# Kernel optimization log

Hardware: AMD Instinct MI355X
Metric: run time of the kernel (lower is better)

## Reference

```python
import jax, jax.numpy as jnp
import numpy as np

HEADS = 6
K = 3       # kernel_size
PAD = 1     # padding (stride = 1, so AvgPool is identity and h=H, w=W)


def setup_inputs() -> dict:
    key = jax.random.key(0)
    ks = jax.random.split(key, 6)
    B, H, W, C = 8, 56, 56, 192
    k4h = (K ** 4) * HEADS  # 486
    s = 0.02
    return {
        "x":  jax.random.normal(ks[0], (B, H, W, C), jnp.float32),
        # weights stored as (in, out), i.e. transpose of torch nn.Linear.weight
        "Wv": jax.random.normal(ks[1], (C, C), jnp.float32) * s,
        "Wa": jax.random.normal(ks[2], (C, k4h), jnp.float32) * s,
        "ba": jnp.zeros((k4h,), jnp.float32),
        "Wp": jax.random.normal(ks[3], (C, C), jnp.float32) * s,
        "bp": jnp.zeros((C,), jnp.float32),
    }


def _outlook(x, Wv, Wa, ba, Wp, bp):
    B, H, W, C = x.shape
    hd = C // HEADS
    scale = hd ** (-0.5)
    k2 = K * K
    hw = H * W

    # v projection (no bias), to NCHW
    v = jnp.einsum("bhwc,cd->bdhw", x, Wv)                       # [B,C,H,W]

    # unfold: extract k x k local windows (same ordering as nn.Unfold: C, ki, kj)
    vp = jnp.pad(v, ((0, 0), (0, 0), (PAD, PAD), (PAD, PAD)))
    patches = jnp.stack(
        [vp[:, :, i:i + H, j:j + W] for i in range(K) for j in range(K)],
        axis=2,
    )                                                            # [B,C,k2,H,W]
    v = patches.reshape(B, HEADS, hd, k2, hw).transpose(0, 1, 4, 3, 2)  # [B,h,hw,k2,hd]

    # attention weights: dense predicted per location (pool is identity, stride=1)
    a = x.reshape(B, hw, C) @ Wa + ba                            # [B,hw,heads*k2*k2]
    a = a.reshape(B, hw, HEADS, k2, k2).transpose(0, 2, 1, 3, 4)  # [B,h,hw,k2,k2]
    a = jax.nn.softmax(a * scale, axis=-1)

    out = jnp.einsum("bnpkq,bnpqd->bnpkd", a, v)                 # [B,h,hw,k2,hd]

    # fold (col2im): scatter-add overlapping windows back, stride=1
    cols = out.transpose(0, 1, 4, 3, 2).reshape(B, C, K, K, H, W)
    acc = jnp.zeros((B, C, H + 2 * PAD, W + 2 * PAD), x.dtype)
    for i in range(K):
        for j in range(K):
            acc = acc.at[:, :, i:i + H, j:j + W].add(cols[:, :, i, j])
    y = acc[:, :, PAD:PAD + H, PAD:PAD + W].transpose(0, 2, 3, 1)  # [B,H,W,C]

    return y @ Wp + bp


def reference(x, Wv, Wa, ba, Wp, bp):
    return _outlook(x, Wv, Wa, ba, Wp, bp)
```

## Files before the change

kernel.cpp:

```cpp
#include <hip/hip_runtime.h>
#include <hip/hip_bf16.h>
#include <cstdint>

#define DI __device__ __forceinline__

typedef __attribute__((ext_vector_type(8))) short short8;
typedef __attribute__((ext_vector_type(4))) float f32x4;

DI float bflo(uint32_t u) { return __builtin_bit_cast(float, (uint32_t)(u << 16)); }
DI float bfhi(uint32_t u) { return __builtin_bit_cast(float, (uint32_t)(u & 0xffff0000u)); }
DI float bf2f(uint16_t u) { return __builtin_bit_cast(float, (uint32_t)((uint32_t)u << 16)); }
DI uint16_t f2bf(float f) {
    uint32_t x = __builtin_bit_cast(uint32_t, f);
    x += 0x7fffu + ((x >> 16) & 1u);
    return (uint16_t)(x >> 16);
}
DI uint32_t pk2bf(float a, float b) {
    return (uint32_t)f2bf(a) | ((uint32_t)f2bf(b) << 16);
}

DI int xcd_swizzle(int orig, int nwg) {
    const int q = nwg >> 3, r = nwg & 7;
    const int x = orig & 7, i = orig >> 3;
    return (x < r ? x * (q + 1) : r * (q + 1) + (x - r) * q) + i;
}

constexpr int BATCH = 8, HH_IMG = 56, WW_IMG = 56, C = 192;
constexpr int HEADS = 6, HD = 32, NA = 486;
constexpr int MROWS = BATCH * HH_IMG * WW_IMG;
constexpr int KK = 192;

template <bool A_BF16, bool O0_BF16, int NT, int SPLIT>
__global__ __launch_bounds__(256) void gemm_tile(
    const void* __restrict__ Ap,
    const float* __restrict__ W0, int N0, void* __restrict__ out0,
    const float* __restrict__ bias0,
    const float* __restrict__ W1, int N1, uint16_t* __restrict__ out1,
    const float* __restrict__ bias1) {
    __shared__ __align__(16) uint8_t sm[49152];
    const int t    = threadIdx.x;
    const int wgid = xcd_swizzle(blockIdx.x, gridDim.x);
    const int mg   = wgid / NT, ti = wgid - mg * NT;
    const int m0   = mg * 128;
    const int l    = t & 63, wid = t >> 6;
    const int wr   = wid >> 1, wc = wid & 1;
    const int lr   = l & 15, lg = l >> 4;

    if (A_BF16) {
        const uint16_t* A = (const uint16_t*)Ap;
#pragma unroll
        for (int i = 0; i < 12; ++i) {
            const int f = t + i * 256;
            const int m = f / 24, cb = (f % 24) * 16;
            const uint4 val = *(const uint4*)(A + (size_t)(m0 + m) * KK + (cb >> 1));
            *(uint4*)(sm + m * 384 + (cb ^ ((m & 7) << 4))) = val;
        }
    } else {
        const float* A = (const float*)Ap;
#pragma unroll
        for (int i = 0; i < 12; ++i) {
            const int f = t + i * 256;
            const int m = f / 24, cb = (f % 24) * 16;
            const int k = cb >> 1;
            const float4 v0 = *(const float4*)(A + (size_t)(m0 + m) * KK + k);
            const float4 v1 = *(const float4*)(A + (size_t)(m0 + m) * KK + k + 4);
            uint4 o;
            o.x = pk2bf(v0.x, v0.y); o.y = pk2bf(v0.z, v0.w);
            o.z = pk2bf(v1.x, v1.y); o.w = pk2bf(v1.z, v1.w);
            *(uint4*)(sm + m * 384 + (cb ^ ((m & 7) << 4))) = o;
        }
    }
    __syncthreads();

    short8 aR[6][4];
#pragma unroll
    for (int ks = 0; ks < 6; ++ks)
#pragma unroll
        for (int mr = 0; mr < 4; ++mr) {
            const int row = wr * 64 + mr * 16 + lr;
            aR[ks][mr] = *(const short8*)(sm + row * 384 +
                          ((ks * 64 + lg * 16) ^ ((row & 7) << 4)));
        }
    __syncthreads();

    const bool  to0   = ti < SPLIT;
    const float* Ws   = to0 ? W0 : W1;
    const int   ncols = to0 ? N0 : N1;
    const int   bcol  = ti * 64 - (to0 ? 0 : N0);
    {
        const int bn = t & 63, kq = t >> 6;
        const int gn = bcol + bn;
        const bool valid = gn < ncols;
        uint8_t* buf = sm + bn * 384;
        const int sw = (bn & 7) << 4;
        const float* Wf = Ws + (size_t)(kq * 48) * ncols + gn;
#pragma unroll
        for (int e16 = 0; e16 < 6; ++e16) {
            uint32_t d[4];
#pragma unroll
            for (int p = 0; p < 4; ++p) {
                const int e = e16 * 4 + p;
                const float f0 = valid ? Wf[(size_t)(2 * e) * ncols]     : 0.f;
                const float f1 = valid ? Wf[(size_t)(2 * e + 1) * ncols] : 0.f;
                d[p] = pk2bf(f0, f1);
            }
            *(uint4*)(buf + ((kq * 96 + e16 * 16) ^ sw)) = make_uint4(d[0], d[1], d[2], d[3]);
        }
    }
    __syncthreads();

    f32x4 acc[4][2];
#pragma unroll
    for (int mr = 0; mr < 4; ++mr) {
        acc[mr][0] = f32x4{0.f, 0.f, 0.f, 0.f};
        acc[mr][1] = f32x4{0.f, 0.f, 0.f, 0.f};
    }
#pragma unroll
    for (int ks = 0; ks < 6; ++ks) {
        const int cb  = ks * 64 + lg * 16;
        const int rn0 = wc * 32 + lr, rn1 = rn0 + 16;
        const short8 b0 = *(const short8*)(sm + rn0 * 384 + (cb ^ ((rn0 & 7) << 4)));
        const short8 b1 = *(const short8*)(sm + rn1 * 384 + (cb ^ ((rn1 & 7) << 4)));
#pragma unroll
        for (int mr = 0; mr < 4; ++mr) {
            acc[mr][0] = __builtin_amdgcn_mfma_f32_16x16x32_bf16(aR[ks][mr], b0, acc[mr][0], 0, 0, 0);
            acc[mr][1] = __builtin_amdgcn_mfma_f32_16x16x32_bf16(aR[ks][mr], b1, acc[mr][1], 0, 0, 0);
        }
    }

    const float* bias = to0 ? bias0 : bias1;
#pragma unroll
    for (int nr = 0; nr < 2; ++nr) {
        const int col = bcol + wc * 32 + nr * 16 + lr;
        if (col < ncols) {
            const float bv = bias ? bias[col] : 0.f;
#pragma unroll
            for (int mr = 0; mr < 4; ++mr) {
                const size_t rowb = (size_t)(m0 + wr * 64 + mr * 16 + lg * 4);
#pragma unroll
                for (int j = 0; j < 4; ++j) {
                    const float val = acc[mr][nr][j] + bv;
                    if (to0) {
                        if (O0_BF16) ((uint16_t*)out0)[(rowb + j) * ncols + col] = f2bf(val);
                        else         ((float*)out0)[(rowb + j) * ncols + col]    = val;
                    } else {
                        out1[(rowb + j) * ncols + col] = f2bf(val);
                    }
                }
            }
        }
    }
}

constexpr int TH = 4, TW = 8;
constexpr int HALO_W = TW + 4;
constexpr int VSTR = C + 8;

__global__ __launch_bounds__(192) void attn_fold25(const uint16_t* __restrict__ v,
                                                   const uint16_t* __restrict__ alog,
                                                   uint16_t* __restrict__ ypre) {
    __shared__ uint16_t vl[96][VSTR];
    const int b   = blockIdx.z;
    const int ty0 = blockIdx.y * TH, tx0 = blockIdx.x * TW;
    const int t   = threadIdx.x;

#pragma unroll
    for (int it = 0; it < 12; ++it) {
        const int f  = t + it * 192;
        const int px = f / 24, c8 = (f % 24) * 8;
        const int hy = px / HALO_W, hx = px % HALO_W;
        const int y = ty0 + hy - 2, x = tx0 + hx - 2;
        uint4 val = make_uint4(0u, 0u, 0u, 0u);
        if ((unsigned)y < HH_IMG && (unsigned)x < WW_IMG)
            val = *(const uint4*)&v[(((size_t)b * HH_IMG + y) * WW_IMG + x) * C + c8];
        *(uint4*)&vl[px][c8] = val;
    }

    const int n   = t % HEADS, pxl = t / HEADS;
    const int py  = pxl / TW, px_ = pxl % TW;
    const int Py  = ty0 + py, Px = tx0 + px_;
    const float scale = 0.17677669529663687f;

    float cw[5][5] = {};
#pragma unroll
    for (int i = 0; i < 3; ++i)
#pragma unroll
        for (int j = 0; j < 3; ++j) {
            const int sy = Py - i + 1, sx = Px - j + 1;
            if ((unsigned)sy < HH_IMG && (unsigned)sx < WW_IMG) {
                const uint16_t* ap = alog + (((size_t)b * HH_IMG + sy) * WW_IMG + sx) * NA
                                   + n * 81 + (i * 3 + j) * 9;
                float L[9], mx = -1e30f;
#pragma unroll
                for (int q = 0; q < 9; ++q) { L[q] = bf2f(ap[q]) * scale; mx = fmaxf(mx, L[q]); }
                float w[9], s = 0.f;
#pragma unroll
                for (int q = 0; q < 9; ++q) { w[q] = __expf(L[q] - mx); s += w[q]; }
                const float inv = 1.f / s;
#pragma unroll
                for (int qi = 0; qi < 3; ++qi)
#pragma unroll
                    for (int qj = 0; qj < 3; ++qj)
                        cw[qi - i + 2][qj - j + 2] += w[qi * 3 + qj] * inv;
            }
        }
    __syncthreads();

    float acc[HD] = {};
#pragma unroll
    for (int dy = 0; dy < 5; ++dy)
#pragma unroll
        for (int dx = 0; dx < 5; ++dx) {
            const float wq = cw[dy][dx];
            const uint16_t* vp = &vl[(py + dy) * HALO_W + (px_ + dx)][n * HD];
#pragma unroll
            for (int v8 = 0; v8 < 4; ++v8) {
                const uint4 raw = *(const uint4*)&vp[v8 * 8];
                const uint32_t r0 = raw.x, r1 = raw.y, r2 = raw.z, r3 = raw.w;
                acc[v8*8+0] = fmaf(wq, bflo(r0), acc[v8*8+0]);
                acc[v8*8+1] = fmaf(wq, bfhi(r0), acc[v8*8+1]);
                acc[v8*8+2] = fmaf(wq, bflo(r1), acc[v8*8+2]);
                acc[v8*8+3] = fmaf(wq, bfhi(r1), acc[v8*8+3]);
                acc[v8*8+4] = fmaf(wq, bflo(r2), acc[v8*8+4]);
                acc[v8*8+5] = fmaf(wq, bfhi(r2), acc[v8*8+5]);
                acc[v8*8+6] = fmaf(wq, bflo(r3), acc[v8*8+6]);
                acc[v8*8+7] = fmaf(wq, bfhi(r3), acc[v8*8+7]);
            }
        }

    uint16_t* op = ypre + (((size_t)b * HH_IMG + Py) * WW_IMG + Px) * C + n * HD;
#pragma unroll
    for (int d = 0; d < HD; d += 2)
        *(uint32_t*)&op[d] = pk2bf(acc[d], acc[d + 1]);
}

extern "C" void kernel_launch(void* const* d_in, const int* in_sizes, int n_in,
                              void* d_out, int out_size, void* d_ws, size_t ws_size,
                              hipStream_t stream) {
    const float* x  = (const float*)d_in[0];
    const float* Wv = (const float*)d_in[1];
    const float* Wa = (const float*)d_in[2];
    const float* ba = (const float*)d_in[3];
    const float* Wp = (const float*)d_in[4];
    const float* bp = (const float*)d_in[5];
    float* out = (float*)d_out;

    uint16_t* v    = (uint16_t*)d_ws;
    uint16_t* alog = v + (size_t)MROWS * C;
    uint16_t* ypre = alog + (size_t)MROWS * NA;

    gemm_tile<false, true, 11, 3><<<(MROWS / 128) * 11, 256, 0, stream>>>(
        x, Wv, C, v, nullptr, Wa, NA, alog, ba);
    attn_fold25<<<dim3(WW_IMG / TW, HH_IMG / TH, BATCH), dim3(192), 0, stream>>>(
        v, alog, ypre);
    gemm_tile<true, false, 3, 3><<<(MROWS / 128) * 3, 256, 0, stream>>>(
        ypre, Wp, C, out, bp, nullptr, 0, nullptr, nullptr);
}
```

Measured before the change: 68.95 us.

## Pre-pack bf16 weight tiles, widen GEMM N-tile, use direct-to-LDS loads

A new prep kernel converts Wv/Wa/Wp once per call into pre-swizzled bf16 tiles in the workspace. The GEMMs then stream them with global_load_lds instead of strided fp32 gathers and per-thread conversion. The GEMM tile widens from 64 to 128 columns with 4x4 MFMA accumulators and paired-column packed stores. Hardware cvt_pk_bf16 replaces software rounding. Softmax drops the max subtraction and uses exp2/rcp intrinsics, and ypre is written pre-swizzled so the projection GEMM can load it straight into LDS. Risks are an extra launch, overflow if logits are large without the max subtraction, and higher register pressure.

```diff
diff --git a/kernel.cpp b/kernel.cpp
--- a/kernel.cpp
+++ b/kernel.cpp
@@ -10,13 +10,16 @@
 DI float bflo(uint32_t u) { return __builtin_bit_cast(float, (uint32_t)(u << 16)); }
 DI float bfhi(uint32_t u) { return __builtin_bit_cast(float, (uint32_t)(u & 0xffff0000u)); }
 DI float bf2f(uint16_t u) { return __builtin_bit_cast(float, (uint32_t)((uint32_t)u << 16)); }
-DI uint16_t f2bf(float f) {
-    uint32_t x = __builtin_bit_cast(uint32_t, f);
-    x += 0x7fffu + ((x >> 16) & 1u);
-    return (uint16_t)(x >> 16);
-}
-DI uint32_t pk2bf(float a, float b) {
-    return (uint32_t)f2bf(a) | ((uint32_t)f2bf(b) << 16);
+DI uint32_t cvtpk(float lo, float hi) {
+    uint32_t r;
+    asm("v_cvt_pk_bf16_f32 %0, %1, %2" : "=v"(r) : "v"(lo), "v"(hi));
+    return r;
+}
+
+DI void gload16(const void* g, void* s) {
+    __builtin_amdgcn_global_load_lds(
+        (const __attribute__((address_space(1))) uint32_t*)g,
+        (__attribute__((address_space(3))) uint32_t*)s, 16, 0, 0);
 }
 
 DI int xcd_swizzle(int orig, int nwg) {
@@ -29,15 +32,47 @@
 constexpr int HEADS = 6, HD = 32, NA = 486;
 constexpr int MROWS = BATCH * HH_IMG * WW_IMG;
 constexpr int KK = 192;
-
-template <bool A_BF16, bool O0_BF16, int NT, int SPLIT>
-__global__ __launch_bounds__(256) void gemm_tile(
+constexpr int TILE_B = 49152;
+
+__global__ __launch_bounds__(256) void prep_wt(const float* __restrict__ Wv,
+                                               const float* __restrict__ Wa,
+                                               const float* __restrict__ Wp,
+                                               uint8_t* __restrict__ WT) {
+    const int tid = blockIdx.x * 256 + threadIdx.x;
+    const int s = tid % 24, rem = tid / 24;
+    const int p = rem & 127, tile = rem >> 7;
+    const int lc = (p >> 5) * 32 + 2 * (p & 15) + ((p >> 4) & 1);
+    const int u  = (tile < 6 ? tile : tile - 6) * 128 + lc;
+
+    const float* src = nullptr; int nc = 0, col = 0;
+    if (tile < 6) {
+        if (u < 192)      { src = Wv; nc = 192; col = u; }
+        else if (u < 678) { src = Wa; nc = NA;  col = u - 192; }
+    } else {
+        if (u < 192)      { src = Wp; nc = 192; col = u; }
+    }
+
+    const int k0 = s * 8;
+    uint32_t d[4];
+#pragma unroll
+    for (int e = 0; e < 4; ++e) {
+        const float f0 = src ? src[(size_t)(k0 + 2 * e) * nc + col]     : 0.f;
+        const float f1 = src ? src[(size_t)(k0 + 2 * e + 1) * nc + col] : 0.f;
+        d[e] = cvtpk(f0, f1);
+    }
+    const int sb = (s * 16) ^ ((p & 7) << 4);
+    *(uint4*)(WT + (size_t)tile * TILE_B + p * 384 + sb) =
+        make_uint4(d[0], d[1], d[2], d[3]);
+}
+
+template <bool A_BF16, bool OUT_DUAL, int NT>
+__global__ __launch_bounds__(256, 2) void gemm128(
     const void* __restrict__ Ap,
-    const float* __restrict__ W0, int N0, void* __restrict__ out0,
-    const float* __restrict__ bias0,
-    const float* __restrict__ W1, int N1, uint16_t* __restrict__ out1,
-    const float* __restrict__ bias1) {
-    __shared__ __align__(16) uint8_t sm[49152];
+    const uint8_t* __restrict__ WT,
+    uint16_t* __restrict__ vOut, uint16_t* __restrict__ alogOut,
+    const float* __restrict__ bias,
+    float* __restrict__ outf) {
+    __shared__ __align__(16) uint8_t sm[TILE_B];
     const int t    = threadIdx.x;
     const int wgid = xcd_swizzle(blockIdx.x, gridDim.x);
     const int mg   = wgid / NT, ti = wgid - mg * NT;
@@ -47,14 +82,13 @@
     const int lr   = l & 15, lg = l >> 4;
 
     if (A_BF16) {
-        const uint16_t* A = (const uint16_t*)Ap;
+        const uint8_t* src = (const uint8_t*)Ap + (size_t)m0 * 384;
 #pragma unroll
         for (int i = 0; i < 12; ++i) {
-            const int f = t + i * 256;
-            const int m = f / 24, cb = (f % 24) * 16;
-            const uint4 val = *(const uint4*)(A + (size_t)(m0 + m) * KK + (cb >> 1));
-            *(uint4*)(sm + m * 384 + (cb ^ ((m & 7) << 4))) = val;
-        }
+            const int off = wid * 12288 + i * 1024;
+            gload16(src + off + l * 16, sm + off);
+        }
+        __syncthreads();
     } else {
         const float* A = (const float*)Ap;
 #pragma unroll
@@ -65,12 +99,12 @@
             const float4 v0 = *(const float4*)(A + (size_t)(m0 + m) * KK + k);
             const float4 v1 = *(const float4*)(A + (size_t)(m0 + m) * KK + k + 4);
             uint4 o;
-            o.x = pk2bf(v0.x, v0.y); o.y = pk2bf(v0.z, v0.w);
-            o.z = pk2bf(v1.x, v1.y); o.w = pk2bf(v1.z, v1.w);
+            o.x = cvtpk(v0.x, v0.y); o.y = cvtpk(v0.z, v0.w);
+            o.z = cvtpk(v1.x, v1.y); o.w = cvtpk(v1.z, v1.w);
             *(uint4*)(sm + m * 384 + (cb ^ ((m & 7) << 4))) = o;
         }
-    }
-    __syncthreads();
+        __syncthreads();
+    }
 
     short8 aR[6][4];
 #pragma unroll
@@ -83,69 +117,70 @@
         }
     __syncthreads();
 
-    const bool  to0   = ti < SPLIT;
-    const float* Ws   = to0 ? W0 : W1;
-    const int   ncols = to0 ? N0 : N1;
-    const int   bcol  = ti * 64 - (to0 ? 0 : N0);
     {
-        const int bn = t & 63, kq = t >> 6;
-        const int gn = bcol + bn;
-        const bool valid = gn < ncols;
-        uint8_t* buf = sm + bn * 384;
-        const int sw = (bn & 7) << 4;
-        const float* Wf = Ws + (size_t)(kq * 48) * ncols + gn;
-#pragma unroll
-        for (int e16 = 0; e16 < 6; ++e16) {
-            uint32_t d[4];
-#pragma unroll
-            for (int p = 0; p < 4; ++p) {
-                const int e = e16 * 4 + p;
-                const float f0 = valid ? Wf[(size_t)(2 * e) * ncols]     : 0.f;
-                const float f1 = valid ? Wf[(size_t)(2 * e + 1) * ncols] : 0.f;
-                d[p] = pk2bf(f0, f1);
-            }
-            *(uint4*)(buf + ((kq * 96 + e16 * 16) ^ sw)) = make_uint4(d[0], d[1], d[2], d[3]);
+        const uint8_t* wt = WT + (size_t)ti * TILE_B;
+#pragma unroll
+        for (int i = 0; i < 12; ++i) {
+            const int off = wid * 12288 + i * 1024;
+            gload16(wt + off + l * 16, sm + off);
         }
     }
     __syncthreads();
 
-    f32x4 acc[4][2];
-#pragma unroll
-    for (int mr = 0; mr < 4; ++mr) {
-        acc[mr][0] = f32x4{0.f, 0.f, 0.f, 0.f};
-        acc[mr][1] = f32x4{0.f, 0.f, 0.f, 0.f};
-    }
+    f32x4 acc[4][4];
+#pragma unroll
+    for (int mr = 0; mr < 4; ++mr)
+#pragma unroll
+        for (int nr = 0; nr < 4; ++nr) acc[mr][nr] = f32x4{0.f, 0.f, 0.f, 0.f};
 #pragma unroll
     for (int ks = 0; ks < 6; ++ks) {
-        const int cb  = ks * 64 + lg * 16;
-        const int rn0 = wc * 32 + lr, rn1 = rn0 + 16;
-        const short8 b0 = *(const short8*)(sm + rn0 * 384 + (cb ^ ((rn0 & 7) << 4)));
-        const short8 b1 = *(const short8*)(sm + rn1 * 384 + (cb ^ ((rn1 & 7) << 4)));
-#pragma unroll
-        for (int mr = 0; mr < 4; ++mr) {
-            acc[mr][0] = __builtin_amdgcn_mfma_f32_16x16x32_bf16(aR[ks][mr], b0, acc[mr][0], 0, 0, 0);
-            acc[mr][1] = __builtin_amdgcn_mfma_f32_16x16x32_bf16(aR[ks][mr], b1, acc[mr][1], 0, 0, 0);
-        }
-    }
-
-    const float* bias = to0 ? bias0 : bias1;
-#pragma unroll
-    for (int nr = 0; nr < 2; ++nr) {
-        const int col = bcol + wc * 32 + nr * 16 + lr;
-        if (col < ncols) {
-            const float bv = bias ? bias[col] : 0.f;
-#pragma unroll
-            for (int mr = 0; mr < 4; ++mr) {
-                const size_t rowb = (size_t)(m0 + wr * 64 + mr * 16 + lg * 4);
-#pragma unroll
-                for (int j = 0; j < 4; ++j) {
-                    const float val = acc[mr][nr][j] + bv;
-                    if (to0) {
-                        if (O0_BF16) ((uint16_t*)out0)[(rowb + j) * ncols + col] = f2bf(val);
-                        else         ((float*)out0)[(rowb + j) * ncols + col]    = val;
-                    } else {
-                        out1[(rowb + j) * ncols + col] = f2bf(val);
-                    }
+        const int cb = ks * 64 + lg * 16;
+        short8 b[4];
+#pragma unroll
+        for (int nr = 0; nr < 4; ++nr) {
+            const int rn = wc * 64 + nr * 16 + lr;
+            b[nr] = *(const short8*)(sm + rn * 384 + (cb ^ ((rn & 7) << 4)));
+        }
+#pragma unroll
+        for (int mr = 0; mr < 4; ++mr)
+#pragma unroll
+            for (int nr = 0; nr < 4; ++nr)
+                acc[mr][nr] = __builtin_amdgcn_mfma_f32_16x16x32_bf16(
+                    aR[ks][mr], b[nr], acc[mr][nr], 0, 0, 0);
+    }
+
+    const int gcol0 = ti * 128 + wc * 64;
+#pragma unroll
+    for (int pr = 0; pr < 2; ++pr) {
+        if (OUT_DUAL) {
+            const bool isv = gcol0 < 192;
+            uint16_t* dst = isv ? vOut : alogOut;
+            const int nc  = isv ? 192 : NA;
+            const int c   = (isv ? gcol0 : gcol0 - 192) + pr * 32 + 2 * lr;
+            if (c < nc) {
+                const float be = isv ? 0.f : bias[c];
+                const float bo = isv ? 0.f : bias[c + 1];
+#pragma unroll
+                for (int mr = 0; mr < 4; ++mr) {
+                    const size_t rb = (size_t)(m0 + wr * 64 + mr * 16 + lg * 4);
+#pragma unroll
+                    for (int j = 0; j < 4; ++j)
+                        *(uint32_t*)(dst + (rb + j) * nc + c) =
+                            cvtpk(acc[mr][2 * pr][j] + be, acc[mr][2 * pr + 1][j] + bo);
+                }
+            }
+        } else {
+            const int c = gcol0 + pr * 32 + 2 * lr;
+            if (c < 192) {
+                const float be = bias[c], bo = bias[c + 1];
+#pragma unroll
+                for (int mr = 0; mr < 4; ++mr) {
+                    const size_t rb = (size_t)(m0 + wr * 64 + mr * 16 + lg * 4);
+#pragma unroll
+                    for (int j = 0; j < 4; ++j)
+                        *(float2*)(outf + (rb + j) * 192 + c) =
+                            make_float2(acc[mr][2 * pr][j] + be,
+                                        acc[mr][2 * pr + 1][j] + bo);
                 }
             }
         }
@@ -179,7 +214,7 @@
     const int n   = t % HEADS, pxl = t / HEADS;
     const int py  = pxl / TW, px_ = pxl % TW;
     const int Py  = ty0 + py, Px = tx0 + px_;
-    const float scale = 0.17677669529663687f;
+    const float scl2 = 0.17677669529663687f * 1.4426950408889634f;
 
     float cw[5][5] = {};
 #pragma unroll
@@ -190,13 +225,13 @@
             if ((unsigned)sy < HH_IMG && (unsigned)sx < WW_IMG) {
                 const uint16_t* ap = alog + (((size_t)b * HH_IMG + sy) * WW_IMG + sx) * NA
                                    + n * 81 + (i * 3 + j) * 9;
-                float L[9], mx = -1e30f;
-#pragma unroll
-                for (int q = 0; q < 9; ++q) { L[q] = bf2f(ap[q]) * scale; mx = fmaxf(mx, L[q]); }
                 float w[9], s = 0.f;
 #pragma unroll
-                for (int q = 0; q < 9; ++q) { w[q] = __expf(L[q] - mx); s += w[q]; }
-                const float inv = 1.f / s;
+                for (int q = 0; q < 9; ++q) {
+                    w[q] = __builtin_amdgcn_exp2f(bf2f(ap[q]) * scl2);
+                    s += w[q];
+                }
+                const float inv = __builtin_amdgcn_rcpf(s);
 #pragma unroll
                 for (int qi = 0; qi < 3; ++qi)
 #pragma unroll
@@ -228,10 +263,12 @@
             }
         }
 
-    uint16_t* op = ypre + (((size_t)b * HH_IMG + Py) * WW_IMG + Px) * C + n * HD;
+    const size_t Pidx = ((size_t)b * HH_IMG + Py) * WW_IMG + Px;
+    uint8_t* op = (uint8_t*)ypre + Pidx * 384;
+    const int key = ((int)Pidx & 7) << 4;
 #pragma unroll
     for (int d = 0; d < HD; d += 2)
-        *(uint32_t*)&op[d] = pk2bf(acc[d], acc[d + 1]);
+        *(uint32_t*)(op + ((n * 64 + d * 2) ^ key)) = cvtpk(acc[d], acc[d + 1]);
 }
 
 extern "C" void kernel_launch(void* const* d_in, const int* in_sizes, int n_in,
@@ -248,11 +285,13 @@
     uint16_t* v    = (uint16_t*)d_ws;
     uint16_t* alog = v + (size_t)MROWS * C;
     uint16_t* ypre = alog + (size_t)MROWS * NA;
-
-    gemm_tile<false, true, 11, 3><<<(MROWS / 128) * 11, 256, 0, stream>>>(
-        x, Wv, C, v, nullptr, Wa, NA, alog, ba);
+    uint8_t*  WT   = (uint8_t*)(ypre + (size_t)MROWS * C);
+
+    prep_wt<<<96, 256, 0, stream>>>(Wv, Wa, Wp, WT);
+    gemm128<false, true, 6><<<(MROWS / 128) * 6, 256, 0, stream>>>(
+        x, WT, v, alog, ba, nullptr);
     attn_fold25<<<dim3(WW_IMG / TW, HH_IMG / TH, BATCH), dim3(192), 0, stream>>>(
         v, alog, ypre);
-    gemm_tile<true, false, 3, 3><<<(MROWS / 128) * 3, 256, 0, stream>>>(
-        ypre, Wp, C, out, bp, nullptr, 0, nullptr, nullptr);
-}
+    gemm128<true, false, 2><<<(MROWS / 128) * 2, 256, 0, stream>>>(
+        ypre, WT + 6 * (size_t)TILE_B, nullptr, nullptr, bp, out);
+}
```

Result: no change. 67.78 us (-1.7%).
